# Performance work log

Measured on AMD Instinct MI355X. Metric: run time of the kernel, lower is better.

Reference implementation:

```python
import jax, jax.numpy as jnp
import numpy as np

B, T, C = 2, 2048, 1024
NH, NKV, HD = 16, 4, 64
THETA = 10000.0


def setup_inputs() -> dict:
    key = jax.random.key(0)
    k1, k2, k3 = jax.random.split(key, 3)
    x = jax.random.normal(k1, (B, T, C), dtype=jnp.float32)
    W_qkv = jax.random.normal(k2, (C, (NH + 2 * NKV) * HD), dtype=jnp.float32) * 0.02
    W_proj = jax.random.normal(k3, (C, C), dtype=jnp.float32) * 0.02
    return {"x": x, "W_qkv": W_qkv, "W_proj": W_proj}


def _rope_tables(t_len):
    inv_freq = 1.0 / (THETA ** (jnp.arange(0, HD, 2, dtype=jnp.float32) / HD))  # [HD/2]
    t = jnp.arange(t_len, dtype=jnp.float32)
    freqs = jnp.outer(t, inv_freq)  # [T, HD/2]
    return jnp.cos(freqs), jnp.sin(freqs)


def _apply_rope(x, cos, sin):
    # x: [B, T, H, D] with interleaved pairs (even/odd lanes)
    x1 = x[..., 0::2]
    x2 = x[..., 1::2]
    cos = cos[None, :, None, :]
    sin = sin[None, :, None, :]
    o1 = x1 * cos - x2 * sin
    o2 = x1 * sin + x2 * cos
    return jnp.stack([o1, o2], axis=-1).reshape(x.shape)


def reference(x, W_qkv, W_proj):
    qkv = x @ W_qkv  # [B, T, (NH+2*NKV)*HD]
    q, k, v = jnp.split(qkv, [NH * HD, NH * HD + NKV * HD], axis=2)
    q = q.reshape(B, T, NH, HD)
    k = k.reshape(B, T, NKV, HD)
    v = v.reshape(B, T, NKV, HD)
    cos, sin = _rope_tables(T)
    q = _apply_rope(q, cos, sin)
    k = _apply_rope(k, cos, sin)
    rep = NH // NKV
    k = jnp.repeat(k, rep, axis=2)  # GQA: [B, T, NH, HD]
    v = jnp.repeat(v, rep, axis=2)
    att = jnp.einsum('bqhd,bkhd->bhqk', q, k) / jnp.sqrt(jnp.float32(HD))
    causal = jnp.tril(jnp.ones((T, T), dtype=bool))
    att = jnp.where(causal[None, None], att, -jnp.inf)
    att = jax.nn.softmax(att, axis=-1)
    y = jnp.einsum('bhqk,bkhd->bqhd', att, v).reshape(B, T, C)
    return y @ W_proj
```

## Files before the change

kernel.cpp:

```cpp
#include <hip/hip_runtime.h>
#include <hip/hip_bf16.h>

#define B_ 2
#define T_ 2048
#define C_ 1024
#define NH_ 16
#define NKV_ 4
#define HD_ 64
#define NQKV_ 1536
#define M_ 4096

typedef __attribute__((ext_vector_type(8))) __bf16 bf16x8;
typedef __attribute__((ext_vector_type(4))) __bf16 bf16x4;
typedef __attribute__((ext_vector_type(4))) float f32x4;
typedef __attribute__((ext_vector_type(4))) unsigned int u32x4;

__device__ __forceinline__ float fast_exp2(float x) { return __builtin_amdgcn_exp2f(x); }

#define GLOAD_LDS16(gptr, lptr)                                                        \
  __builtin_amdgcn_global_load_lds(                                                    \
      (const __attribute__((address_space(1))) unsigned int*)(gptr),                   \
      (__attribute__((address_space(3))) unsigned int*)(lptr), 16, 0, 0)

__device__ __forceinline__ void transpose_tile_body(const float* __restrict__ in,
                                                    __bf16* __restrict__ out,
                                                    int K, int N, int n0, int k0,
                                                    __bf16 (*tile)[72], int tid) {
  const int tr = tid >> 4, tc4 = (tid & 15) << 2;
  #pragma unroll
  for (int p = 0; p < 4; ++p) {
    const int k = k0 + p * 16 + tr;
    const float4 v = *(const float4*)&in[(size_t)k * N + n0 + tc4];
    tile[tc4 + 0][p * 16 + tr] = (__bf16)v.x;
    tile[tc4 + 1][p * 16 + tr] = (__bf16)v.y;
    tile[tc4 + 2][p * 16 + tr] = (__bf16)v.z;
    tile[tc4 + 3][p * 16 + tr] = (__bf16)v.w;
  }
  __syncthreads();
  #pragma unroll
  for (int p = 0; p < 4; ++p) {
    const int n = n0 + p * 16 + tr;
    bf16x4 o;
    o.x = tile[p * 16 + tr][tc4 + 0];
    o.y = tile[p * 16 + tr][tc4 + 1];
    o.z = tile[p * 16 + tr][tc4 + 2];
    o.w = tile[p * 16 + tr][tc4 + 3];
    *(bf16x4*)&out[(size_t)n * K + k0 + tc4] = o;
  }
}

#define NB_CASTX 2048
#define NB_TWQKV 384
#define NB_TWPROJ 256
#define PREP_GRID (NB_CASTX + NB_TWQKV + NB_TWPROJ + 256)
__global__ __launch_bounds__(256) void prep_kernel(const float* __restrict__ x,
                                                   const float* __restrict__ Wqkv,
                                                   const float* __restrict__ Wproj,
                                                   __bf16* __restrict__ xb,
                                                   __bf16* __restrict__ wqkvT,
                                                   __bf16* __restrict__ wprojT,
                                                   float* __restrict__ cosT,
                                                   float* __restrict__ sinT) {
  __shared__ __bf16 tile[64][72];
  const int blk = blockIdx.x, tid = threadIdx.x;
  if (blk < NB_CASTX) {
    const int i = blk * 256 + tid;
    const float4 v0 = ((const float4*)x)[2 * i];
    const float4 v1 = ((const float4*)x)[2 * i + 1];
    bf16x8 o;
    o[0] = (__bf16)v0.x; o[1] = (__bf16)v0.y; o[2] = (__bf16)v0.z; o[3] = (__bf16)v0.w;
    o[4] = (__bf16)v1.x; o[5] = (__bf16)v1.y; o[6] = (__bf16)v1.z; o[7] = (__bf16)v1.w;
    ((bf16x8*)xb)[i] = o;
  } else if (blk < NB_CASTX + NB_TWQKV) {
    const int bx = blk - NB_CASTX;
    transpose_tile_body(Wqkv, wqkvT, C_, NQKV_, (bx % (NQKV_ / 64)) * 64,
                        (bx / (NQKV_ / 64)) * 64, tile, tid);
  } else if (blk < NB_CASTX + NB_TWQKV + NB_TWPROJ) {
    const int bx = blk - NB_CASTX - NB_TWQKV;
    transpose_tile_body(Wproj, wprojT, C_, C_, (bx % (C_ / 64)) * 64,
                        (bx / (C_ / 64)) * 64, tile, tid);
  } else {
    const int idx = (blk - NB_CASTX - NB_TWQKV - NB_TWPROJ) * 256 + tid;
    const int t = idx >> 5, i = idx & 31;
    const float inv = powf(10000.0f, -(float)i * (1.0f / 32.0f));
    const float ang = (float)t * inv;
    cosT[idx] = cosf(ang);
    sinT[idx] = sinf(ang);
  }
}

__global__ __launch_bounds__(256) void gemm_qkv_kernel(const __bf16* __restrict__ A,
                                                       const __bf16* __restrict__ Bt,
                                                       const float* __restrict__ cosT,
                                                       const float* __restrict__ sinT,
                                                       __bf16* __restrict__ Q,
                                                       __bf16* __restrict__ Kb,
                                                       __bf16* __restrict__ Vt) {
  const int N = NQKV_, K = C_;
  __shared__ __align__(16) __bf16 lA[2][128 * 64];
  __shared__ __align__(16) __bf16 lB[2][64 * 64];
  const int tid = threadIdx.x;
  const int lane = tid & 63;
  const int wave = tid >> 6;
  const int wr = wave >> 1, wc = wave & 1;
  const int m0 = blockIdx.y * 128, n0 = blockIdx.x * 64;
  const int srow = tid >> 3, kc = tid & 7;
  const int r16 = lane & 15, g = lane >> 4;
  f32x4 acc[4][2] = {};
  const int nt = K >> 6;

#define GSTAGE(buf, k0)                                                                   \
  {                                                                                       \
    _Pragma("unroll")                                                                     \
    for (int p = 0; p < 4; ++p) {                                                         \
      const int row = p * 32 + srow;                                                      \
      const int sw = (kc ^ (row & 7)) * 8;                                                \
      GLOAD_LDS16(&A[(size_t)(m0 + row) * K + (k0) + sw], &lA[buf][row * 64 + kc * 8]);   \
    }                                                                                     \
    _Pragma("unroll")                                                                     \
    for (int p = 0; p < 2; ++p) {                                                         \
      const int row = p * 32 + srow;                                                      \
      const int sw = (kc ^ (row & 7)) * 8;                                                \
      GLOAD_LDS16(&Bt[(size_t)(n0 + row) * K + (k0) + sw], &lB[buf][row * 64 + kc * 8]);  \
    }                                                                                     \
  }
  GSTAGE(0, 0);
  asm volatile("s_waitcnt vmcnt(0)" ::: "memory");
  __syncthreads();
  int cur = 0;
  for (int t = 0; t < nt; ++t) {
    if (t + 1 < nt) GSTAGE(cur ^ 1, (t + 1) << 6);
    #pragma unroll
    for (int ks = 0; ks < 64; ks += 32) {
      bf16x8 af[4], bfr[2];
      const int kch = (ks >> 3) + g;
      #pragma unroll
      for (int mi = 0; mi < 4; ++mi) {
        const int row = wr * 64 + mi * 16 + r16;
        af[mi] = *(const bf16x8*)&lA[cur][row * 64 + (kch ^ (row & 7)) * 8];
      }
      #pragma unroll
      for (int ni = 0; ni < 2; ++ni) {
        const int row = wc * 32 + ni * 16 + r16;
        bfr[ni] = *(const bf16x8*)&lB[cur][row * 64 + (kch ^ (row & 7)) * 8];
      }
      #pragma unroll
      for (int mi = 0; mi < 4; ++mi)
        #pragma unroll
        for (int ni = 0; ni < 2; ++ni)
          acc[mi][ni] = __builtin_amdgcn_mfma_f32_16x16x32_bf16(af[mi], bfr[ni], acc[mi][ni], 0, 0, 0);
    }
    asm volatile("s_waitcnt vmcnt(0)" ::: "memory");
    __syncthreads();
    cur ^= 1;
  }
#undef GSTAGE
  const int bx = blockIdx.x;
  const bool isV = bx >= 20;
  const bool isQ = bx < 16;
  const float qs = 0.125f * 1.44269504f;
  const bool evenD = (r16 & 1) == 0;
  #pragma unroll
  for (int mi = 0; mi < 4; ++mi) {
    const int t0g = m0 + wr * 64 + mi * 16 + g * 4;
    const int b = t0g >> 11, tq0 = t0g & 2047;
    #pragma unroll
    for (int ni = 0; ni < 2; ++ni) {
      const int d = wc * 32 + ni * 16 + r16;
      if (isV) {
        const int hv = bx - 20;
        bf16x4 o4;
        #pragma unroll
        for (int j = 0; j < 4; ++j) o4[j] = (__bf16)acc[mi][ni][j];
        *(bf16x4*)&Vt[(((size_t)b * NKV_ + hv) * HD_ + d) * T_ + tq0] = o4;
      } else {
        const int ir = d >> 1;
        #pragma unroll
        for (int j = 0; j < 4; ++j) {
          const float val = acc[mi][ni][j];
          const float oth = __shfl_xor(val, 1);
          const float c = cosT[(tq0 + j) * 32 + ir];
          const float s = sinT[(tq0 + j) * 32 + ir];
          float o = evenD ? (val * c - oth * s) : (oth * s + val * c);
          if (isQ) {
            Q[(((size_t)b * NH_ + bx) * T_ + tq0 + j) * HD_ + d] = (__bf16)(o * qs);
          } else {
            Kb[(((size_t)b * NKV_ + (bx - 16)) * T_ + tq0 + j) * HD_ + d] = (__bf16)o;
          }
        }
      }
    }
  }
}

__global__ __launch_bounds__(256) void gemm_tn_kernel(const __bf16* __restrict__ A,
                                                      const __bf16* __restrict__ Bt,
                                                      float* __restrict__ C, int N, int K) {
  __shared__ __align__(16) __bf16 lA[2][128 * 64];
  __shared__ __align__(16) __bf16 lB[2][64 * 64];
  const int tid = threadIdx.x;
  const int lane = tid & 63;
  const int wave = tid >> 6;
  const int wr = wave >> 1, wc = wave & 1;
  const int m0 = blockIdx.y * 128, n0 = blockIdx.x * 64;
  const int srow = tid >> 3, kc = tid & 7;
  const int r16 = lane & 15, g = lane >> 4;
  f32x4 acc[4][2] = {};
  const int nt = K >> 6;

#define GSTAGE(buf, k0)                                                                   \
  {                                                                                       \
    _Pragma("unroll")                                                                     \
    for (int p = 0; p < 4; ++p) {                                                         \
      const int row = p * 32 + srow;                                                      \
      const int sw = (kc ^ (row & 7)) * 8;                                                \
      GLOAD_LDS16(&A[(size_t)(m0 + row) * K + (k0) + sw], &lA[buf][row * 64 + kc * 8]);   \
    }                                                                                     \
    _Pragma("unroll")                                                                     \
    for (int p = 0; p < 2; ++p) {                                                         \
      const int row = p * 32 + srow;                                                      \
      const int sw = (kc ^ (row & 7)) * 8;                                                \
      GLOAD_LDS16(&Bt[(size_t)(n0 + row) * K + (k0) + sw], &lB[buf][row * 64 + kc * 8]);  \
    }                                                                                     \
  }
  GSTAGE(0, 0);
  asm volatile("s_waitcnt vmcnt(0)" ::: "memory");
  __syncthreads();
  int cur = 0;
  for (int t = 0; t < nt; ++t) {
    if (t + 1 < nt) GSTAGE(cur ^ 1, (t + 1) << 6);
    #pragma unroll
    for (int ks = 0; ks < 64; ks += 32) {
      bf16x8 af[4], bfr[2];
      const int kch = (ks >> 3) + g;
      #pragma unroll
      for (int mi = 0; mi < 4; ++mi) {
        const int row = wr * 64 + mi * 16 + r16;
        af[mi] = *(const bf16x8*)&lA[cur][row * 64 + (kch ^ (row & 7)) * 8];
      }
      #pragma unroll
      for (int ni = 0; ni < 2; ++ni) {
        const int row = wc * 32 + ni * 16 + r16;
        bfr[ni] = *(const bf16x8*)&lB[cur][row * 64 + (kch ^ (row & 7)) * 8];
      }
      #pragma unroll
      for (int mi = 0; mi < 4; ++mi)
        #pragma unroll
        for (int ni = 0; ni < 2; ++ni)
          acc[mi][ni] = __builtin_amdgcn_mfma_f32_16x16x32_bf16(af[mi], bfr[ni], acc[mi][ni], 0, 0, 0);
    }
    asm volatile("s_waitcnt vmcnt(0)" ::: "memory");
    __syncthreads();
    cur ^= 1;
  }
  #pragma unroll
  for (int mi = 0; mi < 4; ++mi) {
    const int r0 = m0 + wr * 64 + mi * 16 + g * 4;
    #pragma unroll
    for (int ni = 0; ni < 2; ++ni) {
      const int c = n0 + wc * 32 + ni * 16 + r16;
      #pragma unroll
      for (int j = 0; j < 4; ++j)
        C[(size_t)(r0 + j) * N + c] = acc[mi][ni][j];
    }
  }
#undef GSTAGE
}

__global__ __launch_bounds__(256) void attn_kernel(const __bf16* __restrict__ Q,
                                                   const __bf16* __restrict__ Kb,
                                                   const __bf16* __restrict__ Vt,
                                                   __bf16* __restrict__ Y) {
  __shared__ __align__(16) __bf16 lK[2][128 * 64];
  __shared__ __align__(16) __bf16 lV[2][64 * 128];
  __shared__ __align__(16) __bf16 pP[4][16 * 128];
  const int tid = threadIdx.x;
  const int lane = tid & 63, wave = tid >> 6;
  const int r16 = lane & 15, g = lane >> 4;
  const int logical = (blockIdx.x & 7) * 64 + (blockIdx.x >> 3);
  const int i = logical & 15;
  const int bh = logical >> 4;
  const int b = bh >> 4, h = bh & 15;
  const int kvh = h >> 2;
  const __bf16* Qp = Q + ((size_t)b * NH_ + h) * T_ * HD_;
  const __bf16* Kp = Kb + ((size_t)b * NKV_ + kvh) * T_ * HD_;
  const __bf16* Vp = Vt + ((size_t)b * NKV_ + kvh) * HD_ * T_;
  const int qtile[2] = { i, 31 - i };
  const int srow = tid >> 3, kc = tid & 7;
  const int vrow = tid >> 4, vkc = tid & 15;

#define ASTAGE(buf, kv0_)                                                                  \
  {                                                                                        \
    _Pragma("unroll")                                                                      \
    for (int p = 0; p < 4; ++p) {                                                          \
      const int row = p * 32 + srow;                                                       \
      const int sw = (kc ^ (row & 7)) * 8;                                                 \
      GLOAD_LDS16(&Kp[(size_t)((kv0_) + row) * HD_ + sw], &lK[buf][row * 64 + kc * 8]);    \
    }                                                                                      \
    _Pragma("unroll")                                                                      \
    for (int p = 0; p < 4; ++p) {                                                          \
      const int d = p * 16 + vrow;                                                         \
      const int ch = vkc ^ (d & 7);                                                        \
      GLOAD_LDS16(&Vp[(size_t)d * T_ + (kv0_) + ch * 8], &lV[buf][d * 128 + vkc * 8]);     \
    }                                                                                      \
  }

  bf16x8 qf[2][2];
  #pragma unroll
  for (int sd = 0; sd < 2; ++sd)
    #pragma unroll
    for (int c = 0; c < 2; ++c)
      qf[sd][c] = *(const bf16x8*)&Qp[(size_t)(qtile[sd] * 64 + wave * 16 + r16) * HD_ + (c * 4 + g) * 8];

  f32x4 o[2][4] = {};
  float mS[2], lS[2];
  #pragma unroll
  for (int sd = 0; sd < 2; ++sd) { mS[sd] = -__builtin_inff(); lS[sd] = 0.0f; }

  auto sm_side = [&](f32x4 (&s)[8], int sd) {
    f32x4 v4 = s[0];
    #pragma unroll
    for (int ni = 1; ni < 8; ++ni)
      #pragma unroll
      for (int j = 0; j < 4; ++j) v4[j] = fmaxf(v4[j], s[ni][j]);
    float pm = fmaxf(fmaxf(v4[0], v4[1]), fmaxf(v4[2], v4[3]));
    pm = fmaxf(pm, __shfl_xor(pm, 16));
    pm = fmaxf(pm, __shfl_xor(pm, 32));
    const bool upd = pm > mS[sd] + 8.0f;
    const float nm = upd ? pm : mS[sd];
    const float sc = fast_exp2(mS[sd] - nm);
    mS[sd] = nm;
    lS[sd] *= sc;
    if (__any(upd)) {
      #pragma unroll
      for (int j = 0; j < 4; ++j) {
        const float scj = __shfl(sc, g * 4 + j);
        #pragma unroll
        for (int nf = 0; nf < 4; ++nf) o[sd][nf][j] *= scj;
      }
    }
    float rs = 0.0f;
    #pragma unroll
    for (int ni = 0; ni < 8; ++ni) {
      bf16x4 pb;
      #pragma unroll
      for (int j = 0; j < 4; ++j) {
        const float pv = fast_exp2(s[ni][j] - mS[sd]);
        rs += pv;
        pb[j] = (__bf16)pv;
      }
      const int ch = 2 * ni + (g >> 1);
      *(bf16x4*)&pP[wave][r16 * 128 + ((ch ^ (r16 & 15)) * 8) + (g & 1) * 4] = pb;
    }
    rs += __shfl_xor(rs, 16);
    rs += __shfl_xor(rs, 32);
    lS[sd] += rs;
  };

  const int ntiles = (33 - i) >> 1;
  const int diagA = i >> 1;
  ASTAGE(0, 0);
  asm volatile("s_waitcnt vmcnt(0)" ::: "memory");
  __syncthreads();
  int cur = 0;

  for (int t = 0; t < ntiles; ++t) {
    const int kv0 = t << 7;
    if (t + 1 < ntiles) ASTAGE(cur ^ 1, kv0 + 128);

    #pragma unroll
    for (int sd = 0; sd < 2; ++sd) {
      if (sd == 0 && t > diagA) continue;
      const int qw = qtile[sd] * 64 + wave * 16;

      f32x4 s[8] = {};
      #pragma unroll
      for (int c = 0; c < 2; ++c)
        #pragma unroll
        for (int ni = 0; ni < 8; ++ni) {
          const int row = ni * 16 + r16;
          const bf16x8 kf = *(const bf16x8*)&lK[cur][row * 64 + ((c * 4 + g) ^ (row & 7)) * 8];
          s[ni] = __builtin_amdgcn_mfma_f32_16x16x32_bf16(kf, qf[sd][c], s[ni], 0, 0, 0);
        }

      if (t == ((sd == 0) ? diagA : (ntiles - 1))) {
        #pragma unroll
        for (int ni = 0; ni < 8; ++ni)
          #pragma unroll
          for (int j = 0; j < 4; ++j)
            if (kv0 + ni * 16 + g * 4 + j > qw + r16) s[ni][j] = -__builtin_inff();
      }

      sm_side(s, sd);
      asm volatile("s_waitcnt lgkmcnt(0)" ::: "memory");

      #pragma unroll
      for (int c = 0; c < 4; ++c) {
        const bf16x8 pf = *(const bf16x8*)&pP[wave][r16 * 128 + (((c * 4 + g) ^ (r16 & 15)) * 8)];
        #pragma unroll
        for (int nf = 0; nf < 4; ++nf) {
          const int row = nf * 16 + r16;
          const bf16x8 vf = *(const bf16x8*)&lV[cur][row * 128 + ((c * 4 + g) ^ (row & 7)) * 8];
          o[sd][nf] = __builtin_amdgcn_mfma_f32_16x16x32_bf16(pf, vf, o[sd][nf], 0, 0, 0);
        }
      }
    }

    asm volatile("s_waitcnt vmcnt(0)" ::: "memory");
    __syncthreads();
    cur ^= 1;
  }

  #pragma unroll
  for (int sd = 0; sd < 2; ++sd) {
    const int qw = qtile[sd] * 64 + wave * 16;
    #pragma unroll
    for (int j = 0; j < 4; ++j) {
      const float lq = __shfl(lS[sd], g * 4 + j);
      const float inv = 1.0f / lq;
      const int tq = qw + g * 4 + j;
      #pragma unroll
      for (int nf = 0; nf < 4; ++nf) {
        const int d = nf * 16 + r16;
        Y[(((size_t)b * T_ + tq) * NH_ + h) * HD_ + d] = (__bf16)(o[sd][nf][j] * inv);
      }
    }
  }
#undef ASTAGE
}

extern "C" void kernel_launch(void* const* d_in, const int* in_sizes, int n_in,
                              void* d_out, int out_size, void* d_ws, size_t ws_size,
                              hipStream_t stream) {
  const float* x = (const float*)d_in[0];
  const float* Wqkv = (const float*)d_in[1];
  const float* Wproj = (const float*)d_in[2];
  float* out = (float*)d_out;

  char* ws = (char*)d_ws;
  size_t off = 0;
  auto alloc = [&](size_t bytes) {
    char* p = ws + off;
    off += (bytes + 255) & ~(size_t)255;
    return p;
  };
  __bf16* xb     = (__bf16*)alloc((size_t)M_ * C_ * 2);
  __bf16* wqkvT  = (__bf16*)alloc((size_t)NQKV_ * C_ * 2);
  __bf16* wprojT = (__bf16*)alloc((size_t)C_ * C_ * 2);
  float*  cosT   = (float*)alloc((size_t)T_ * 32 * 4);
  float*  sinT   = (float*)alloc((size_t)T_ * 32 * 4);
  __bf16* Qb     = (__bf16*)alloc((size_t)B_ * NH_ * T_ * HD_ * 2);
  __bf16* Kb     = (__bf16*)alloc((size_t)B_ * NKV_ * T_ * HD_ * 2);
  __bf16* Vt     = (__bf16*)alloc((size_t)B_ * NKV_ * T_ * HD_ * 2);
  __bf16* Yb     = (__bf16*)alloc((size_t)M_ * C_ * 2);

  hipLaunchKernelGGL(prep_kernel, dim3(PREP_GRID), dim3(256), 0, stream,
                     x, Wqkv, Wproj, xb, wqkvT, wprojT, cosT, sinT);
  hipLaunchKernelGGL(gemm_qkv_kernel, dim3(NQKV_ / 64, M_ / 128), dim3(256), 0, stream,
                     xb, wqkvT, cosT, sinT, Qb, Kb, Vt);
  hipLaunchKernelGGL(attn_kernel, dim3(16 * B_ * NH_), dim3(256), 0, stream, Qb, Kb, Vt, Yb);
  hipLaunchKernelGGL(gemm_tn_kernel, dim3(C_ / 64, M_ / 128), dim3(256), 0, stream,
                     Yb, wprojT, out, C_, C_);
}
```

Baseline: 111.9 us.

## Shrink attention KV tile to 64 and hoist K/V fragments across both query sides

Reduces the KV tile from 128 to 64 keys per iteration, which halves the LDS footprint for K, V and P and doubles the number of loop iterations. K and V fragments are now read from LDS once per tile and reused for both query tiles, where before each side reloaded them. The causal diagonal logic and swizzles are adjusted to the new tile size. In exchange there are more barriers and softmax rescale steps per key, and more registers held for the hoisted fragments.

```diff
diff --git a/kernel.cpp b/kernel.cpp
--- a/kernel.cpp
+++ b/kernel.cpp
@@ -271,9 +271,9 @@
                                                    const __bf16* __restrict__ Kb,
                                                    const __bf16* __restrict__ Vt,
                                                    __bf16* __restrict__ Y) {
-  __shared__ __align__(16) __bf16 lK[2][128 * 64];
-  __shared__ __align__(16) __bf16 lV[2][64 * 128];
-  __shared__ __align__(16) __bf16 pP[4][16 * 128];
+  __shared__ __align__(16) __bf16 lK[2][64 * 64];
+  __shared__ __align__(16) __bf16 lV[2][64 * 64];
+  __shared__ __align__(16) __bf16 pP[4][16 * 64];
   const int tid = threadIdx.x;
   const int lane = tid & 63, wave = tid >> 6;
   const int r16 = lane & 15, g = lane >> 4;
@@ -287,21 +287,15 @@
   const __bf16* Vp = Vt + ((size_t)b * NKV_ + kvh) * HD_ * T_;
   const int qtile[2] = { i, 31 - i };
   const int srow = tid >> 3, kc = tid & 7;
-  const int vrow = tid >> 4, vkc = tid & 15;
 
 #define ASTAGE(buf, kv0_)                                                                  \
   {                                                                                        \
     _Pragma("unroll")                                                                      \
-    for (int p = 0; p < 4; ++p) {                                                          \
+    for (int p = 0; p < 2; ++p) {                                                          \
       const int row = p * 32 + srow;                                                       \
       const int sw = (kc ^ (row & 7)) * 8;                                                 \
       GLOAD_LDS16(&Kp[(size_t)((kv0_) + row) * HD_ + sw], &lK[buf][row * 64 + kc * 8]);    \
-    }                                                                                      \
-    _Pragma("unroll")                                                                      \
-    for (int p = 0; p < 4; ++p) {                                                          \
-      const int d = p * 16 + vrow;                                                         \
-      const int ch = vkc ^ (d & 7);                                                        \
-      GLOAD_LDS16(&Vp[(size_t)d * T_ + (kv0_) + ch * 8], &lV[buf][d * 128 + vkc * 8]);     \
+      GLOAD_LDS16(&Vp[(size_t)row * T_ + (kv0_) + sw], &lV[buf][row * 64 + kc * 8]);       \
     }                                                                                      \
   }
 
@@ -317,13 +311,15 @@
   #pragma unroll
   for (int sd = 0; sd < 2; ++sd) { mS[sd] = -__builtin_inff(); lS[sd] = 0.0f; }
 
-  auto sm_side = [&](f32x4 (&s)[8], int sd) {
-    f32x4 v4 = s[0];
-    #pragma unroll
-    for (int ni = 1; ni < 8; ++ni)
-      #pragma unroll
-      for (int j = 0; j < 4; ++j) v4[j] = fmaxf(v4[j], s[ni][j]);
-    float pm = fmaxf(fmaxf(v4[0], v4[1]), fmaxf(v4[2], v4[3]));
+  auto sm_side = [&](f32x4 (&s)[4], int sd) {
+    float t0 = fmaxf(fmaxf(s[0][0], s[0][1]), s[0][2]);
+    float t1 = fmaxf(fmaxf(s[0][3], s[1][0]), s[1][1]);
+    float t2 = fmaxf(fmaxf(s[1][2], s[1][3]), s[2][0]);
+    float t3 = fmaxf(fmaxf(s[2][1], s[2][2]), s[2][3]);
+    float t4 = fmaxf(fmaxf(s[3][0], s[3][1]), s[3][2]);
+    float pm = fmaxf(fmaxf(t0, t1), t2);
+    pm = fmaxf(pm, fmaxf(t3, t4));
+    pm = fmaxf(pm, s[3][3]);
     pm = fmaxf(pm, __shfl_xor(pm, 16));
     pm = fmaxf(pm, __shfl_xor(pm, 32));
     const bool upd = pm > mS[sd] + 8.0f;
@@ -341,7 +337,7 @@
     }
     float rs = 0.0f;
     #pragma unroll
-    for (int ni = 0; ni < 8; ++ni) {
+    for (int ni = 0; ni < 4; ++ni) {
       bf16x4 pb;
       #pragma unroll
       for (int j = 0; j < 4; ++j) {
@@ -350,42 +346,49 @@
         pb[j] = (__bf16)pv;
       }
       const int ch = 2 * ni + (g >> 1);
-      *(bf16x4*)&pP[wave][r16 * 128 + ((ch ^ (r16 & 15)) * 8) + (g & 1) * 4] = pb;
+      *(bf16x4*)&pP[wave][r16 * 64 + ((ch ^ (r16 & 7)) * 8) + (g & 1) * 4] = pb;
     }
     rs += __shfl_xor(rs, 16);
     rs += __shfl_xor(rs, 32);
     lS[sd] += rs;
   };
 
-  const int ntiles = (33 - i) >> 1;
-  const int diagA = i >> 1;
+  const int ntiles = 32 - i;
   ASTAGE(0, 0);
   asm volatile("s_waitcnt vmcnt(0)" ::: "memory");
   __syncthreads();
   int cur = 0;
 
   for (int t = 0; t < ntiles; ++t) {
-    const int kv0 = t << 7;
-    if (t + 1 < ntiles) ASTAGE(cur ^ 1, kv0 + 128);
+    const int kv0 = t << 6;
+    if (t + 1 < ntiles) ASTAGE(cur ^ 1, kv0 + 64);
+
+    bf16x8 kf[2][4], vf[2][4];
+    #pragma unroll
+    for (int c = 0; c < 2; ++c)
+      #pragma unroll
+      for (int ni = 0; ni < 4; ++ni) {
+        const int row = ni * 16 + r16;
+        const int sw = ((c * 4 + g) ^ (row & 7)) * 8;
+        kf[c][ni] = *(const bf16x8*)&lK[cur][row * 64 + sw];
+        vf[c][ni] = *(const bf16x8*)&lV[cur][row * 64 + sw];
+      }
 
     #pragma unroll
     for (int sd = 0; sd < 2; ++sd) {
-      if (sd == 0 && t > diagA) continue;
+      if (sd == 0 && t > i) continue;
       const int qw = qtile[sd] * 64 + wave * 16;
 
-      f32x4 s[8] = {};
+      f32x4 s[4] = {};
       #pragma unroll
       for (int c = 0; c < 2; ++c)
         #pragma unroll
-        for (int ni = 0; ni < 8; ++ni) {
-          const int row = ni * 16 + r16;
-          const bf16x8 kf = *(const bf16x8*)&lK[cur][row * 64 + ((c * 4 + g) ^ (row & 7)) * 8];
-          s[ni] = __builtin_amdgcn_mfma_f32_16x16x32_bf16(kf, qf[sd][c], s[ni], 0, 0, 0);
-        }
-
-      if (t == ((sd == 0) ? diagA : (ntiles - 1))) {
-        #pragma unroll
-        for (int ni = 0; ni < 8; ++ni)
+        for (int ni = 0; ni < 4; ++ni)
+          s[ni] = __builtin_amdgcn_mfma_f32_16x16x32_bf16(kf[c][ni], qf[sd][c], s[ni], 0, 0, 0);
+
+      if (t == ((sd == 0) ? i : (ntiles - 1))) {
+        #pragma unroll
+        for (int ni = 0; ni < 4; ++ni)
           #pragma unroll
           for (int j = 0; j < 4; ++j)
             if (kv0 + ni * 16 + g * 4 + j > qw + r16) s[ni][j] = -__builtin_inff();
@@ -395,14 +398,11 @@
       asm volatile("s_waitcnt lgkmcnt(0)" ::: "memory");
 
       #pragma unroll
-      for (int c = 0; c < 4; ++c) {
-        const bf16x8 pf = *(const bf16x8*)&pP[wave][r16 * 128 + (((c * 4 + g) ^ (r16 & 15)) * 8)];
-        #pragma unroll
-        for (int nf = 0; nf < 4; ++nf) {
-          const int row = nf * 16 + r16;
-          const bf16x8 vf = *(const bf16x8*)&lV[cur][row * 128 + ((c * 4 + g) ^ (row & 7)) * 8];
-          o[sd][nf] = __builtin_amdgcn_mfma_f32_16x16x32_bf16(pf, vf, o[sd][nf], 0, 0, 0);
-        }
+      for (int c = 0; c < 2; ++c) {
+        const bf16x8 pf = *(const bf16x8*)&pP[wave][r16 * 64 + (((c * 4 + g) ^ (r16 & 7)) * 8)];
+        #pragma unroll
+        for (int nf = 0; nf < 4; ++nf)
+          o[sd][nf] = __builtin_amdgcn_mfma_f32_16x16x32_bf16(pf, vf[c][nf], o[sd][nf], 0, 0, 0);
       }
     }
 
```

Result: faster. 95.67 us (median of 2 runs) (-14.5%).
